# Kernel tuning notes

Measured on AMD Instinct MI355X. Metric: run time of the kernel, lower is better.

## Reference

```python
import jax, jax.numpy as jnp
import numpy as np
import math

POWER = 4
NUM_LEVELS = 2
STDS = [8, 4, 2, 1]          # stds sorted descending, as in __init__
KSIZE = 31                    # max(stds)*4 - 1
MAX_MIP = (NUM_LEVELS - 1) + math.log(2 * max(STDS)) / math.log(POWER)  # 3.0


def _blur_kernel():
    # (12, 3, 31, 31): output channel 3*i+c is a Gaussian(std=STDS[i]) applied to input channel c
    d = np.arange(KSIZE, dtype=np.float64) - (KSIZE - 1) / 2.0
    K = np.zeros((3 * len(STDS), 3, KSIZE, KSIZE), np.float32)
    for i, s in enumerate(STDS):
        g1 = np.exp(-0.5 * (d / s) ** 2)
        g1 = g1 / g1.sum()
        g = np.outer(g1, g1).astype(np.float32)
        for c in range(3):
            K[3 * i + c, c] = g
    return jnp.asarray(K)


def cube_sample(tex, dirs):
    # tex: (6, H, W, 3) cubemap faces in OpenGL order (+x,-x,+y,-y,+z,-z); dirs: (B, 3)
    H, W = tex.shape[1], tex.shape[2]
    x, y, z = dirs[:, 0], dirs[:, 1], dirs[:, 2]
    ax, ay, az = jnp.abs(x), jnp.abs(y), jnp.abs(z)
    is_x = (ax >= ay) & (ax >= az)
    is_y = (~is_x) & (ay >= az)
    face = jnp.where(is_x, jnp.where(x >= 0, 0, 1),
                     jnp.where(is_y, jnp.where(y >= 0, 2, 3),
                               jnp.where(z >= 0, 4, 5)))
    ma = jnp.where(is_x, ax, jnp.where(is_y, ay, az))
    conds = [face == i for i in range(6)]
    sc = jnp.select(conds, [-z, z, x, x, x, -x])
    tc = jnp.select(conds, [-y, -y, z, -z, -y, -y])
    inv = 1.0 / jnp.maximum(ma, 1e-12)
    u = 0.5 * (sc * inv + 1.0)
    v = 0.5 * (tc * inv + 1.0)
    fx = u * W - 0.5
    fy = v * H - 0.5
    x0 = jnp.floor(fx)
    y0 = jnp.floor(fy)
    wx = (fx - x0)[:, None]
    wy = (fy - y0)[:, None]
    x0i = jnp.clip(x0, 0, W - 1).astype(jnp.int32)
    x1i = jnp.clip(x0 + 1, 0, W - 1).astype(jnp.int32)
    y0i = jnp.clip(y0, 0, H - 1).astype(jnp.int32)
    y1i = jnp.clip(y0 + 1, 0, H - 1).astype(jnp.int32)
    t00 = tex[face, y0i, x0i]
    t10 = tex[face, y0i, x1i]
    t01 = tex[face, y1i, x0i]
    t11 = tex[face, y1i, x1i]
    return ((t00 * (1 - wx) + t10 * wx) * (1 - wy)
            + (t01 * (1 - wx) + t11 * wx) * wy)


def setup_inputs() -> dict:
    key = jax.random.key(0)
    k1, k2, k3, k4 = jax.random.split(key, 4)
    B = 2097152
    res = 512
    viewdirs = jax.random.normal(k1, (B, 3), dtype=jnp.float32)
    viewdirs = viewdirs / jnp.linalg.norm(viewdirs, axis=-1, keepdims=True)
    # miplevel = log(saSample/saTexel)/log(4)/2 ; make it span [0, 3.2] so the mask path fires
    saTexel = 4.0 * math.pi / (6 * res * res)
    u = jax.random.uniform(k2, (B, 1), dtype=jnp.float32)
    saSample = saTexel * (float(POWER) ** (2.0 * 3.2 * u))
    # learned cubemaps: coarse (128) then fine (512), as in bg_mats list order
    bg_mat0 = 0.1 + 0.05 * jax.random.normal(k3, (6, 128, 128, 3), dtype=jnp.float32)
    bg_mat1 = 0.1 + 0.05 * jax.random.normal(k4, (6, 512, 512, 3), dtype=jnp.float32)
    return {"viewdirs": viewdirs, "saSample": saSample, "bg_mat0": bg_mat0, "bg_mat1": bg_mat1}


def reference(viewdirs, saSample, bg_mat0, bg_mat1):
    res = bg_mat1.shape[1]
    saTexel = 4.0 * math.pi / (6 * res * res)
    miplevel = jnp.clip(jnp.log(saSample / saTexel) / math.log(POWER) / 2.0, 0.0, MAX_MIP)  # (B,1)

    # main level pass: mip=1 (coarse, weight 1/(2-1)=1), mip=0 (fine, weight 1/2)
    img = cube_sample(bg_mat0, viewdirs) * 1.0 + cube_sample(bg_mat1, viewdirs) * 0.5

    # blur pyramid from coarse map (start_mip=1, weight=1, identity activation)
    faces = jnp.transpose(bg_mat0, (0, 3, 1, 2))  # (6,3,h,h)
    conv = jax.lax.conv_general_dilated(faces, _blur_kernel(), (1, 1), 'SAME',
                                        dimension_numbers=('NCHW', 'OIHW', 'NCHW'))
    blur = jnp.zeros_like(img)
    wsum = jnp.zeros_like(miplevel)
    for i, s in enumerate(STDS):
        mat = jnp.transpose(conv[:, 3 * i:3 * i + 3], (0, 2, 3, 1))  # (6,h,h,3)
        mip = (NUM_LEVELS - 1) + math.log(2 * s) / math.log(POWER)
        w = 1.0 - jnp.clip(jnp.abs(mip - miplevel), 0.0, 1.0)  # (B,1)
        blur = blur + cube_sample(mat, viewdirs) * w
        wsum = wsum + w
    mask = miplevel >= NUM_LEVELS  # (B,1)
    img = jnp.where(mask, blur / jnp.maximum(wsum, 1e-8), img)
    return img
```

## Files before the change

kernel.cpp:

```cpp
#include <hip/hip_runtime.h>
#include <hip/hip_fp16.h>
#include <math.h>

#define KSIZE 31
#define HRAD 15

#define QSCALE (1023.0f / 0.75f)
#define QINV   (0.75f / 1023.0f)
#define QOFF   0.25f

union H8U { float4 f4; __half h[8]; };

__device__ inline unsigned quant3(float r, float g, float b) {
    int qr = (int)((r + QOFF) * QSCALE + 0.5f);
    int qg = (int)((g + QOFF) * QSCALE + 0.5f);
    int qb = (int)((b + QOFF) * QSCALE + 0.5f);
    qr = min(max(qr, 0), 1023);
    qg = min(max(qg, 0), 1023);
    qb = min(max(qb, 0), 1023);
    return (unsigned)(qr | (qg << 10) | (qb << 20));
}

__device__ inline float deqc(unsigned q, int sh) {
    return (float)((q >> sh) & 1023u) * QINV - QOFF;
}

__device__ inline void cube_coords(float x, float y, float z,
                                   int& face, float& u, float& v) {
    float ax = fabsf(x), ay = fabsf(y), az = fabsf(z);
    bool is_x = (ax >= ay) && (ax >= az);
    bool is_y = (!is_x) && (ay >= az);
    float ma, sc, tc;
    if (is_x) {
        if (x >= 0.0f) { face = 0; sc = -z; } else { face = 1; sc = z; }
        ma = ax; tc = -y;
    } else if (is_y) {
        if (y >= 0.0f) { face = 2; tc = z; } else { face = 3; tc = -z; }
        ma = ay; sc = x;
    } else {
        if (z >= 0.0f) { face = 4; sc = x; } else { face = 5; sc = -x; }
        ma = az; tc = -y;
    }
    float inv = 1.0f / fmaxf(ma, 1e-12f);
    u = 0.5 * (sc * inv + 1.0f);
    v = 0.5 * (tc * inv + 1.0f);
}

__device__ inline void nbq_setup(float u, float v, int HW, int face,
                                 int& rec, float& wx, float& wy) {
    float fx = u * (float)HW - 0.5f;
    float fy = v * (float)HW - 0.5f;
    float x0 = floorf(fx), y0 = floorf(fy);
    wx = fx - x0;
    wy = fy - y0;
    int xi = (int)x0, yi = (int)y0;
    if (xi < 0) { xi = 0; wx = 0.0f; }
    if (yi < 0) { yi = 0; wy = 0.0f; }
    rec = (face * HW + yi) * HW + xi;
}

__device__ inline void weights_inline(int tid, float wS[4][32]) {
    const float ss[4] = {8.f, 4.f, 2.f, 1.f};
    int lvl = (tid >> 5) & 3;
    int tap = tid & 31;
    float d = (float)tap - 15.0f;
    float q = d / ss[lvl];
    float g = (tap < KSIZE) ? expf(-0.5f * q * q) : 0.0f;
    float s = g;
#pragma unroll
    for (int k = 16; k; k >>= 1) s += __shfl_xor(s, k, 32);
    if (tid < 128) wS[lvl][tap] = g / s;
}

__global__ __launch_bounds__(256)
void prep1(const float* __restrict__ bg0, const float* __restrict__ bg1,
           float4* __restrict__ tmpH, uint4* __restrict__ bg0q,
           uint4* __restrict__ bg1q) {
    __shared__ float sm[1664];
    int b = blockIdx.x;
    int tid = threadIdx.x;

    if (b < 6144) {
        float* smA = sm;
        float* smB = sm + 771;
        int half = b & 1;
        int y    = (b >> 1) & 511;
        int f    = b >> 10;
        int x0   = half * 256;
        int yn   = min(y + 1, 511);
        const float* rowA = bg1 + (size_t)(f * 512 + y)  * 1536;
        const float* rowB = bg1 + (size_t)(f * 512 + yn) * 1536;
        for (int k = tid; k < 771; k += 256) {
            int t = k / 3;
            int c = k - t * 3;
            int gx = min(x0 + t, 511);
            smA[k] = rowA[gx * 3 + c];
            smB[k] = rowB[gx * 3 + c];
        }
        __syncthreads();
        int t0 = tid * 3;
        uint4 r;
        r.x = quant3(smA[t0 + 0], smA[t0 + 1], smA[t0 + 2]);
        r.y = quant3(smA[t0 + 3], smA[t0 + 4], smA[t0 + 5]);
        r.z = quant3(smB[t0 + 0], smB[t0 + 1], smB[t0 + 2]);
        r.w = quant3(smB[t0 + 3], smB[t0 + 4], smB[t0 + 5]);
        bg1q[(size_t)(f * 512 + y) * 512 + x0 + tid] = r;
        return;
    }

    float (*rows)[2][384] = (float (*)[2][384])sm;
    float (*wS)[32] = (float (*)[32])(sm + 1536);

    int bid  = b - 6144;
    int unit = tid >> 7;
    int lane = tid & 127;
    int face = bid / 64;
    int yrow = (bid % 64) * 2 + unit;

    weights_inline(tid, wS);

    int ynext = min(yrow + 1, 127);
    const float* srcA = bg0 + (size_t)(face * 128 + yrow) * 384;
    const float* srcB = bg0 + (size_t)(face * 128 + ynext) * 384;
    for (int k = lane; k < 384; k += 128) {
        rows[unit][0][k] = srcA[k];
        rows[unit][1][k] = srcB[k];
    }
    __syncthreads();

    int x = lane;
    float a[4][3] = {};
    for (int t = 0; t < KSIZE; ++t) {
        int xx = x + t - HRAD;
        if (xx >= 0 && xx < 128) {
            float r0 = rows[unit][0][xx * 3 + 0];
            float r1 = rows[unit][0][xx * 3 + 1];
            float r2 = rows[unit][0][xx * 3 + 2];
#pragma unroll
            for (int l = 0; l < 4; ++l) {
                float w = wS[l][t];
                a[l][0] += w * r0; a[l][1] += w * r1; a[l][2] += w * r2;
            }
        }
    }
    size_t idx = (size_t)(face * 128 + yrow) * 128 + x;
    H8U ta, tb;
#pragma unroll
    for (int l = 0; l < 2; ++l) {
        ta.h[l * 4 + 0] = __float2half(a[l][0]);
        ta.h[l * 4 + 1] = __float2half(a[l][1]);
        ta.h[l * 4 + 2] = __float2half(a[l][2]);
        ta.h[l * 4 + 3] = __float2half(0.0f);
        tb.h[l * 4 + 0] = __float2half(a[2 + l][0]);
        tb.h[l * 4 + 1] = __float2half(a[2 + l][1]);
        tb.h[l * 4 + 2] = __float2half(a[2 + l][2]);
        tb.h[l * 4 + 3] = __float2half(0.0f);
    }
    tmpH[idx * 2 + 0] = ta.f4;
    tmpH[idx * 2 + 1] = tb.f4;

    int x1 = min(x + 1, 127);
    uint4 r;
    r.x = quant3(rows[unit][0][x * 3 + 0], rows[unit][0][x * 3 + 1], rows[unit][0][x * 3 + 2]);
    r.y = quant3(rows[unit][0][x1 * 3 + 0], rows[unit][0][x1 * 3 + 1], rows[unit][0][x1 * 3 + 2]);
    r.z = quant3(rows[unit][1][x * 3 + 0], rows[unit][1][x * 3 + 1], rows[unit][1][x * 3 + 2]);
    r.w = quant3(rows[unit][1][x1 * 3 + 0], rows[unit][1][x1 * 3 + 1], rows[unit][1][x1 * 3 + 2]);
    bg0q[idx] = r;
}

__global__ __launch_bounds__(128)
void blur_v4(const float4* __restrict__ tmpH, uint4* __restrict__ blurq) {
    __shared__ float wS[4][32];
    int bid  = blockIdx.x;
    int yrow = bid & 127;
    int face = bid >> 7;
    int tid  = threadIdx.x;

    weights_inline(tid, wS);
    __syncthreads();

    int x = tid;
    float acc[12] = {};
    int ylo = max(yrow - HRAD, 0);
    int yhi = min(yrow + HRAD, 127);
    for (int yy = ylo; yy <= yhi; ++yy) {
        int t = yy - yrow + HRAD;
        size_t idx = (size_t)(face * 128 + yy) * 128 + x;
        H8U qa, qb;
        qa.f4 = tmpH[idx * 2 + 0];
        qb.f4 = tmpH[idx * 2 + 1];
        float w0 = wS[0][t], w1 = wS[1][t], w2 = wS[2][t], w3 = wS[3][t];
        acc[0]  += w0 * __half2float(qa.h[0]);
        acc[1]  += w0 * __half2float(qa.h[1]);
        acc[2]  += w0 * __half2float(qa.h[2]);
        acc[3]  += w1 * __half2float(qa.h[4]);
        acc[4]  += w1 * __half2float(qa.h[5]);
        acc[5]  += w1 * __half2float(qa.h[6]);
        acc[6]  += w2 * __half2float(qb.h[0]);
        acc[7]  += w2 * __half2float(qb.h[1]);
        acc[8]  += w2 * __half2float(qb.h[2]);
        acc[9]  += w3 * __half2float(qb.h[4]);
        acc[10] += w3 * __half2float(qb.h[5]);
        acc[11] += w3 * __half2float(qb.h[6]);
    }

    uint4 r;
    r.x = quant3(acc[0], acc[1], acc[2]);
    r.y = quant3(acc[3], acc[4], acc[5]);
    r.z = quant3(acc[6], acc[7], acc[8]);
    r.w = quant3(acc[9], acc[10], acc[11]);
    blurq[(size_t)(face * 128 + yrow) * 128 + x] = r;
}

__device__ inline void shade_one(float x, float y, float z, float sa,
                                 const uint4* __restrict__ bg0q,
                                 const uint4* __restrict__ bg1q,
                                 const uint4* __restrict__ blurq,
                                 float* __restrict__ R) {
    int face; float u, v;
    cube_coords(x, y, z, face, u, v);

    const float saTexel = (float)(4.0 * M_PI / (6.0 * 512.0 * 512.0));
    float m = logf(sa / saTexel);
    m = m / 1.3862943611198906f;
    m = m * 0.5f;
    m = fminf(fmaxf(m, 0.0f), 3.0f);

    if (m >= 2.0f) {
        float fx = u * 128.0f - 0.5f;
        float fy = v * 128.0f - 0.5f;
        float xf = floorf(fx), yf = floorf(fy);
        float wx = fx - xf, wy = fy - yf;
        int x0i = min(max((int)xf, 0), 127);
        int x1i = min(max((int)xf + 1, 0), 127);
        int y0i = min(max((int)yf, 0), 127);
        int y1i = min(max((int)yf + 1, 0), 127);
        int base = face << 14;
        uint4 q00 = blurq[base + y0i * 128 + x0i];
        uint4 q10 = blurq[base + y0i * 128 + x1i];
        uint4 q01 = blurq[base + y1i * 128 + x0i];
        uint4 q11 = blurq[base + y1i * 128 + x1i];

        float w0 = 1.0f - fminf(fabsf(3.0f - m), 1.0f);
        float w1 = 1.0f - fminf(fabsf(2.5f - m), 1.0f);
        float w2 = 1.0f - fminf(fabsf(2.0f - m), 1.0f);
        float w3 = 1.0f - fminf(fabsf(1.5f - m), 1.0f);
        float inv = 1.0f / fmaxf(w0 + w1 + w2 + w3, 1e-8f);

#pragma unroll
        for (int c = 0; c < 3; ++c) {
            int sh = c * 10;
            float v00 = w0 * deqc(q00.x, sh) + w1 * deqc(q00.y, sh) +
                        w2 * deqc(q00.z, sh) + w3 * deqc(q00.w, sh);
            float v10 = w0 * deqc(q10.x, sh) + w1 * deqc(q10.y, sh) +
                        w2 * deqc(q10.z, sh) + w3 * deqc(q10.w, sh);
            float v01 = w0 * deqc(q01.x, sh) + w1 * deqc(q01.y, sh) +
                        w2 * deqc(q01.z, sh) + w3 * deqc(q01.w, sh);
            float v11 = w0 * deqc(q11.x, sh) + w1 * deqc(q11.y, sh) +
                        w2 * deqc(q11.z, sh) + w3 * deqc(q11.w, sh);
            float top = v00 * (1.0f - wx) + v10 * wx;
            float bot = v01 * (1.0f - wx) + v11 * wx;
            R[c] = (top * (1.0f - wy) + bot * wy) * inv;
        }
    } else {
        int r0; float wx0, wy0;
        nbq_setup(u, v, 128, face, r0, wx0, wy0);
        int r1; float wx1, wy1;
        nbq_setup(u, v, 512, face, r1, wx1, wy1);
        uint4 p0 = bg0q[r0];
        uint4 p1 = bg1q[r1];
#pragma unroll
        for (int c = 0; c < 3; ++c) {
            int sh = c * 10;
            float t0 = deqc(p0.x, sh) * (1.0f - wx0) + deqc(p0.y, sh) * wx0;
            float b0 = deqc(p0.z, sh) * (1.0f - wx0) + deqc(p0.w, sh) * wx0;
            float c0 = t0 * (1.0f - wy0) + b0 * wy0;
            float t1 = deqc(p1.x, sh) * (1.0f - wx1) + deqc(p1.y, sh) * wx1;
            float b1 = deqc(p1.z, sh) * (1.0f - wx1) + deqc(p1.w, sh) * wx1;
            float c1 = t1 * (1.0f - wy1) + b1 * wy1;
            R[c] = c0 + 0.5f * c1;
        }
    }
}

__global__ __launch_bounds__(256)
void shade4(const float4* __restrict__ vd4, const float4* __restrict__ sa4,
            const uint4* __restrict__ bg0q, const uint4* __restrict__ bg1q,
            const uint4* __restrict__ blurq, float4* __restrict__ out4,
            int nquads) {
    int q = blockIdx.x * blockDim.x + threadIdx.x;
    if (q >= nquads) return;

    float4 a = vd4[3 * q + 0];
    float4 b = vd4[3 * q + 1];
    float4 c = vd4[3 * q + 2];
    float4 s = sa4[q];

    float X[4] = {a.x, a.w, b.z, c.y};
    float Y[4] = {a.y, b.x, b.w, c.z};
    float Z[4] = {a.z, b.y, c.x, c.w};
    float S[4] = {s.x, s.y, s.z, s.w};

    float R[12];
#pragma unroll
    for (int r = 0; r < 4; ++r) {
        shade_one(X[r], Y[r], Z[r], S[r], bg0q, bg1q, blurq, &R[3 * r]);
    }

    out4[3 * q + 0] = make_float4(R[0], R[1], R[2],  R[3]);
    out4[3 * q + 1] = make_float4(R[4], R[5], R[6],  R[7]);
    out4[3 * q + 2] = make_float4(R[8], R[9], R[10], R[11]);
}

extern "C" void kernel_launch(void* const* d_in, const int* in_sizes, int n_in,
                              void* d_out, int out_size, void* d_ws, size_t ws_size,
                              hipStream_t stream) {
    const float* viewdirs = (const float*)d_in[0];
    const float* saSample = (const float*)d_in[1];
    const float* bg0      = (const float*)d_in[2];
    const float* bg1      = (const float*)d_in[3];
    float* out = (float*)d_out;

    int B = in_sizes[0] / 3;
    int nquads = B / 4;

    uint4*  blurq = (uint4*)d_ws;
    uint4*  bg0q  = blurq + 98304;
    uint4*  bg1q  = bg0q + 98304;
    float4* tmpH  = (float4*)(bg1q + 1572864);

    prep1<<<6528, 256, 0, stream>>>(bg0, bg1, tmpH, bg0q, bg1q);
    blur_v4<<<6 * 128, 128, 0, stream>>>(tmpH, blurq);

    int blocks = (nquads + 255) / 256;
    shade4<<<blocks, 256, 0, stream>>>((const float4*)viewdirs,
                                       (const float4*)saSample,
                                       bg0q, bg1q, blurq,
                                       (float4*)out, nquads);
}
```

Before: 82.15 us.

## Fuse separable blur passes into one prep kernel with row-tiled shared memory

```diff
diff --git a/kernel.cpp b/kernel.cpp
--- a/kernel.cpp
+++ b/kernel.cpp
@@ -1,5 +1,4 @@
 #include <hip/hip_runtime.h>
-#include <hip/hip_fp16.h>
 #include <math.h>
 
 #define KSIZE 31
@@ -8,8 +7,6 @@
 #define QSCALE (1023.0f / 0.75f)
 #define QINV   (0.75f / 1023.0f)
 #define QOFF   0.25f
-
-union H8U { float4 f4; __half h[8]; };
 
 __device__ inline unsigned quant3(float r, float g, float b) {
     int qr = (int)((r + QOFF) * QSCALE + 0.5f);
@@ -42,8 +39,8 @@
         ma = az; tc = -y;
     }
     float inv = 1.0f / fmaxf(ma, 1e-12f);
-    u = 0.5 * (sc * inv + 1.0f);
-    v = 0.5 * (tc * inv + 1.0f);
+    u = 0.5f * (sc * inv + 1.0f);
+    v = 0.5f * (tc * inv + 1.0f);
 }
 
 __device__ inline void nbq_setup(float u, float v, int HW, int face,
@@ -73,143 +70,119 @@
 }
 
 __global__ __launch_bounds__(256)
-void prep1(const float* __restrict__ bg0, const float* __restrict__ bg1,
-           float4* __restrict__ tmpH, uint4* __restrict__ bg0q,
-           uint4* __restrict__ bg1q) {
-    __shared__ float sm[1664];
+void prep(const float* __restrict__ bg0, const float* __restrict__ bg1,
+          uint4* __restrict__ bg0q, uint4* __restrict__ bg1q,
+          uint4* __restrict__ blurq) {
+    __shared__ float4 sm4[3680];
+    float* sm = (float*)sm4;
     int b = blockIdx.x;
     int tid = threadIdx.x;
 
-    if (b < 6144) {
-        float* smA = sm;
-        float* smB = sm + 771;
-        int half = b & 1;
-        int y    = (b >> 1) & 511;
-        int f    = b >> 10;
-        int x0   = half * 256;
-        int yn   = min(y + 1, 511);
-        const float* rowA = bg1 + (size_t)(f * 512 + y)  * 1536;
-        const float* rowB = bg1 + (size_t)(f * 512 + yn) * 1536;
-        for (int k = tid; k < 771; k += 256) {
-            int t = k / 3;
-            int c = k - t * 3;
-            int gx = min(x0 + t, 511);
-            smA[k] = rowA[gx * 3 + c];
-            smB[k] = rowB[gx * 3 + c];
+    if (b < 384) {
+        int face  = b / 64;
+        int ytile = (b % 64) * 8;
+        for (int i = tid; i < 9 * 384; i += 256) {
+            int r  = i / 384;
+            int c4 = i - r * 384;
+            int gy = min(ytile + r, 511);
+            sm4[r * 384 + c4] =
+                ((const float4*)(bg1 + (size_t)(face * 512 + gy) * 1536))[c4];
         }
         __syncthreads();
-        int t0 = tid * 3;
-        uint4 r;
-        r.x = quant3(smA[t0 + 0], smA[t0 + 1], smA[t0 + 2]);
-        r.y = quant3(smA[t0 + 3], smA[t0 + 4], smA[t0 + 5]);
-        r.z = quant3(smB[t0 + 0], smB[t0 + 1], smB[t0 + 2]);
-        r.w = quant3(smB[t0 + 3], smB[t0 + 4], smB[t0 + 5]);
-        bg1q[(size_t)(f * 512 + y) * 512 + x0 + tid] = r;
+#pragma unroll
+        for (int i = 0; i < 16; ++i) {
+            int idx = i * 256 + tid;
+            int yl  = idx >> 9;
+            int x   = idx & 511;
+            int x1  = min(x + 1, 511);
+            const float* rA = sm + (size_t)yl * 1536;
+            const float* rB = sm + (size_t)(yl + 1) * 1536;
+            uint4 r;
+            r.x = quant3(rA[x * 3 + 0], rA[x * 3 + 1], rA[x * 3 + 2]);
+            r.y = quant3(rA[x1 * 3 + 0], rA[x1 * 3 + 1], rA[x1 * 3 + 2]);
+            r.z = quant3(rB[x * 3 + 0], rB[x * 3 + 1], rB[x * 3 + 2]);
+            r.w = quant3(rB[x1 * 3 + 0], rB[x1 * 3 + 1], rB[x1 * 3 + 2]);
+            bg1q[(size_t)(face * 512 + ytile + yl) * 512 + x] = r;
+        }
         return;
     }
 
-    float (*rows)[2][384] = (float (*)[2][384])sm;
-    float (*wS)[32] = (float (*)[32])(sm + 1536);
-
-    int bid  = b - 6144;
-    int unit = tid >> 7;
-    int lane = tid & 127;
-    int face = bid / 64;
-    int yrow = (bid % 64) * 2 + unit;
+    float (*wS)[32] = (float (*)[32])(sm + 14592);
+    int bb    = b - 384;
+    int face  = bb / 16;
+    int ytile = (bb % 16) * 8;
+    int x     = tid & 127;
+    int half  = tid >> 7;
 
     weights_inline(tid, wS);
 
-    int ynext = min(yrow + 1, 127);
-    const float* srcA = bg0 + (size_t)(face * 128 + yrow) * 384;
-    const float* srcB = bg0 + (size_t)(face * 128 + ynext) * 384;
-    for (int k = lane; k < 384; k += 128) {
-        rows[unit][0][k] = srcA[k];
-        rows[unit][1][k] = srcB[k];
+    for (int i = tid; i < 38 * 96; i += 256) {
+        int r  = i / 96;
+        int c4 = i - r * 96;
+        int gy = ytile - 15 + r;
+        float4 v = make_float4(0.f, 0.f, 0.f, 0.f);
+        if (gy >= 0 && gy <= 127)
+            v = ((const float4*)(bg0 + (size_t)(face * 128 + gy) * 384))[c4];
+        sm4[r * 96 + c4] = v;
     }
     __syncthreads();
 
-    int x = lane;
-    float a[4][3] = {};
-    for (int t = 0; t < KSIZE; ++t) {
-        int xx = x + t - HRAD;
-        if (xx >= 0 && xx < 128) {
-            float r0 = rows[unit][0][xx * 3 + 0];
-            float r1 = rows[unit][0][xx * 3 + 1];
-            float r2 = rows[unit][0][xx * 3 + 2];
-#pragma unroll
-            for (int l = 0; l < 4; ++l) {
-                float w = wS[l][t];
-                a[l][0] += w * r0; a[l][1] += w * r1; a[l][2] += w * r2;
+    int r0 = half * 4;
+    float acc[4][12] = {};
+    for (int rr = 0; rr < 34; ++rr) {
+        int r = r0 + rr;
+        const float* row = sm + (size_t)r * 384;
+        float hv[12] = {};
+        for (int t = 0; t < KSIZE; ++t) {
+            int xx = x + t - HRAD;
+            if (xx >= 0 && xx < 128) {
+                float c0 = row[xx * 3 + 0];
+                float c1 = row[xx * 3 + 1];
+                float c2 = row[xx * 3 + 2];
+#pragma unroll
+                for (int l = 0; l < 4; ++l) {
+                    float w = wS[l][t];
+                    hv[l * 3 + 0] += w * c0;
+                    hv[l * 3 + 1] += w * c1;
+                    hv[l * 3 + 2] += w * c2;
+                }
             }
         }
-    }
-    size_t idx = (size_t)(face * 128 + yrow) * 128 + x;
-    H8U ta, tb;
-#pragma unroll
-    for (int l = 0; l < 2; ++l) {
-        ta.h[l * 4 + 0] = __float2half(a[l][0]);
-        ta.h[l * 4 + 1] = __float2half(a[l][1]);
-        ta.h[l * 4 + 2] = __float2half(a[l][2]);
-        ta.h[l * 4 + 3] = __float2half(0.0f);
-        tb.h[l * 4 + 0] = __float2half(a[2 + l][0]);
-        tb.h[l * 4 + 1] = __float2half(a[2 + l][1]);
-        tb.h[l * 4 + 2] = __float2half(a[2 + l][2]);
-        tb.h[l * 4 + 3] = __float2half(0.0f);
-    }
-    tmpH[idx * 2 + 0] = ta.f4;
-    tmpH[idx * 2 + 1] = tb.f4;
-
-    int x1 = min(x + 1, 127);
-    uint4 r;
-    r.x = quant3(rows[unit][0][x * 3 + 0], rows[unit][0][x * 3 + 1], rows[unit][0][x * 3 + 2]);
-    r.y = quant3(rows[unit][0][x1 * 3 + 0], rows[unit][0][x1 * 3 + 1], rows[unit][0][x1 * 3 + 2]);
-    r.z = quant3(rows[unit][1][x * 3 + 0], rows[unit][1][x * 3 + 1], rows[unit][1][x * 3 + 2]);
-    r.w = quant3(rows[unit][1][x1 * 3 + 0], rows[unit][1][x1 * 3 + 1], rows[unit][1][x1 * 3 + 2]);
-    bg0q[idx] = r;
-}
-
-__global__ __launch_bounds__(128)
-void blur_v4(const float4* __restrict__ tmpH, uint4* __restrict__ blurq) {
-    __shared__ float wS[4][32];
-    int bid  = blockIdx.x;
-    int yrow = bid & 127;
-    int face = bid >> 7;
-    int tid  = threadIdx.x;
-
-    weights_inline(tid, wS);
-    __syncthreads();
-
-    int x = tid;
-    float acc[12] = {};
-    int ylo = max(yrow - HRAD, 0);
-    int yhi = min(yrow + HRAD, 127);
-    for (int yy = ylo; yy <= yhi; ++yy) {
-        int t = yy - yrow + HRAD;
-        size_t idx = (size_t)(face * 128 + yy) * 128 + x;
-        H8U qa, qb;
-        qa.f4 = tmpH[idx * 2 + 0];
-        qb.f4 = tmpH[idx * 2 + 1];
-        float w0 = wS[0][t], w1 = wS[1][t], w2 = wS[2][t], w3 = wS[3][t];
-        acc[0]  += w0 * __half2float(qa.h[0]);
-        acc[1]  += w0 * __half2float(qa.h[1]);
-        acc[2]  += w0 * __half2float(qa.h[2]);
-        acc[3]  += w1 * __half2float(qa.h[4]);
-        acc[4]  += w1 * __half2float(qa.h[5]);
-        acc[5]  += w1 * __half2float(qa.h[6]);
-        acc[6]  += w2 * __half2float(qb.h[0]);
-        acc[7]  += w2 * __half2float(qb.h[1]);
-        acc[8]  += w2 * __half2float(qb.h[2]);
-        acc[9]  += w3 * __half2float(qb.h[4]);
-        acc[10] += w3 * __half2float(qb.h[5]);
-        acc[11] += w3 * __half2float(qb.h[6]);
-    }
-
-    uint4 r;
-    r.x = quant3(acc[0], acc[1], acc[2]);
-    r.y = quant3(acc[3], acc[4], acc[5]);
-    r.z = quant3(acc[6], acc[7], acc[8]);
-    r.w = quant3(acc[9], acc[10], acc[11]);
-    blurq[(size_t)(face * 128 + yrow) * 128 + x] = r;
+#pragma unroll
+        for (int o = 0; o < 4; ++o) {
+            int t = r - (r0 + o);
+            if (t >= 0 && t <= 30) {
+                float w0 = wS[0][t], w1 = wS[1][t], w2 = wS[2][t], w3 = wS[3][t];
+                acc[o][0]  += w0 * hv[0];  acc[o][1]  += w0 * hv[1];  acc[o][2]  += w0 * hv[2];
+                acc[o][3]  += w1 * hv[3];  acc[o][4]  += w1 * hv[4];  acc[o][5]  += w1 * hv[5];
+                acc[o][6]  += w2 * hv[6];  acc[o][7]  += w2 * hv[7];  acc[o][8]  += w2 * hv[8];
+                acc[o][9]  += w3 * hv[9];  acc[o][10] += w3 * hv[10]; acc[o][11] += w3 * hv[11];
+            }
+        }
+    }
+
+#pragma unroll
+    for (int o = 0; o < 4; ++o) {
+        int yl = r0 + o;
+        int y  = ytile + yl;
+        uint4 q;
+        q.x = quant3(acc[o][0], acc[o][1], acc[o][2]);
+        q.y = quant3(acc[o][3], acc[o][4], acc[o][5]);
+        q.z = quant3(acc[o][6], acc[o][7], acc[o][8]);
+        q.w = quant3(acc[o][9], acc[o][10], acc[o][11]);
+        blurq[(size_t)(face * 128 + y) * 128 + x] = q;
+
+        const float* rowY  = sm + (size_t)(15 + yl) * 384;
+        int yl1 = (y < 127) ? (15 + yl + 1) : (15 + yl);
+        const float* rowY1 = sm + (size_t)yl1 * 384;
+        int x1 = min(x + 1, 127);
+        uint4 p;
+        p.x = quant3(rowY[x * 3 + 0],  rowY[x * 3 + 1],  rowY[x * 3 + 2]);
+        p.y = quant3(rowY[x1 * 3 + 0], rowY[x1 * 3 + 1], rowY[x1 * 3 + 2]);
+        p.z = quant3(rowY1[x * 3 + 0],  rowY1[x * 3 + 1],  rowY1[x * 3 + 2]);
+        p.w = quant3(rowY1[x1 * 3 + 0], rowY1[x1 * 3 + 1], rowY1[x1 * 3 + 2]);
+        bg0q[(size_t)(face * 128 + y) * 128 + x] = p;
+    }
 }
 
 __device__ inline void shade_one(float x, float y, float z, float sa,
@@ -324,13 +297,11 @@
     int B = in_sizes[0] / 3;
     int nquads = B / 4;
 
-    uint4*  blurq = (uint4*)d_ws;
-    uint4*  bg0q  = blurq + 98304;
-    uint4*  bg1q  = bg0q + 98304;
-    float4* tmpH  = (float4*)(bg1q + 1572864);
-
-    prep1<<<6528, 256, 0, stream>>>(bg0, bg1, tmpH, bg0q, bg1q);
-    blur_v4<<<6 * 128, 128, 0, stream>>>(tmpH, blurq);
+    uint4* blurq = (uint4*)d_ws;
+    uint4* bg0q  = blurq + 98304;
+    uint4* bg1q  = bg0q + 98304;
+
+    prep<<<480, 256, 0, stream>>>(bg0, bg1, bg0q, bg1q, blurq);
 
     int blocks = (nquads + 255) / 256;
     shade4<<<blocks, 256, 0, stream>>>((const float4*)viewdirs,
```

New measurement: 172.2 us. 110% more time.

## Rebalance prep kernels: overlap bg1 packing with vertical blur, split blur per half

Applied to the files above, without the earlier changes.

```diff
diff --git a/kernel.cpp b/kernel.cpp
--- a/kernel.cpp
+++ b/kernel.cpp
@@ -42,8 +42,8 @@
         ma = az; tc = -y;
     }
     float inv = 1.0f / fmaxf(ma, 1e-12f);
-    u = 0.5 * (sc * inv + 1.0f);
-    v = 0.5 * (tc * inv + 1.0f);
+    u = 0.5f * (sc * inv + 1.0f);
+    v = 0.5f * (tc * inv + 1.0f);
 }
 
 __device__ inline void nbq_setup(float u, float v, int HW, int face,
@@ -73,45 +73,14 @@
 }
 
 __global__ __launch_bounds__(256)
-void prep1(const float* __restrict__ bg0, const float* __restrict__ bg1,
-           float4* __restrict__ tmpH, uint4* __restrict__ bg0q,
-           uint4* __restrict__ bg1q) {
+void hblur(const float* __restrict__ bg0, float4* __restrict__ tmpH,
+           uint4* __restrict__ bg0q) {
     __shared__ float sm[1664];
-    int b = blockIdx.x;
-    int tid = threadIdx.x;
-
-    if (b < 6144) {
-        float* smA = sm;
-        float* smB = sm + 771;
-        int half = b & 1;
-        int y    = (b >> 1) & 511;
-        int f    = b >> 10;
-        int x0   = half * 256;
-        int yn   = min(y + 1, 511);
-        const float* rowA = bg1 + (size_t)(f * 512 + y)  * 1536;
-        const float* rowB = bg1 + (size_t)(f * 512 + yn) * 1536;
-        for (int k = tid; k < 771; k += 256) {
-            int t = k / 3;
-            int c = k - t * 3;
-            int gx = min(x0 + t, 511);
-            smA[k] = rowA[gx * 3 + c];
-            smB[k] = rowB[gx * 3 + c];
-        }
-        __syncthreads();
-        int t0 = tid * 3;
-        uint4 r;
-        r.x = quant3(smA[t0 + 0], smA[t0 + 1], smA[t0 + 2]);
-        r.y = quant3(smA[t0 + 3], smA[t0 + 4], smA[t0 + 5]);
-        r.z = quant3(smB[t0 + 0], smB[t0 + 1], smB[t0 + 2]);
-        r.w = quant3(smB[t0 + 3], smB[t0 + 4], smB[t0 + 5]);
-        bg1q[(size_t)(f * 512 + y) * 512 + x0 + tid] = r;
-        return;
-    }
-
     float (*rows)[2][384] = (float (*)[2][384])sm;
     float (*wS)[32] = (float (*)[32])(sm + 1536);
 
-    int bid  = b - 6144;
+    int bid  = blockIdx.x;
+    int tid  = threadIdx.x;
     int unit = tid >> 7;
     int lane = tid & 127;
     int face = bid / 64;
@@ -168,48 +137,71 @@
     bg0q[idx] = r;
 }
 
-__global__ __launch_bounds__(128)
-void blur_v4(const float4* __restrict__ tmpH, uint4* __restrict__ blurq) {
-    __shared__ float wS[4][32];
-    int bid  = blockIdx.x;
-    int yrow = bid & 127;
-    int face = bid >> 7;
-    int tid  = threadIdx.x;
+__global__ __launch_bounds__(256)
+void packv(const float* __restrict__ bg1, const float4* __restrict__ tmpH,
+           uint4* __restrict__ bg1q, uint2* __restrict__ blurq2) {
+    __shared__ float4 sm4[768];
+    int b = blockIdx.x;
+    int tid = threadIdx.x;
+
+    if (b < 3072) {
+        float* sm = (float*)sm4;
+        int y    = b & 511;
+        int face = b >> 9;
+        int yn   = min(y + 1, 511);
+        const float4* rA = (const float4*)(bg1 + (size_t)(face * 512 + y)  * 1536);
+        const float4* rB = (const float4*)(bg1 + (size_t)(face * 512 + yn) * 1536);
+        for (int i = tid; i < 384; i += 256) {
+            sm4[i]       = rA[i];
+            sm4[384 + i] = rB[i];
+        }
+        __syncthreads();
+        const float* a  = sm;
+        const float* bb = sm + 1536;
+#pragma unroll
+        for (int e = 0; e < 2; ++e) {
+            int x  = e * 256 + tid;
+            int x1 = min(x + 1, 511);
+            uint4 r;
+            r.x = quant3(a[x * 3 + 0],  a[x * 3 + 1],  a[x * 3 + 2]);
+            r.y = quant3(a[x1 * 3 + 0], a[x1 * 3 + 1], a[x1 * 3 + 2]);
+            r.z = quant3(bb[x * 3 + 0],  bb[x * 3 + 1],  bb[x * 3 + 2]);
+            r.w = quant3(bb[x1 * 3 + 0], bb[x1 * 3 + 1], bb[x1 * 3 + 2]);
+            bg1q[(size_t)(face * 512 + y) * 512 + x] = r;
+        }
+        return;
+    }
+
+    float (*wS)[32] = (float (*)[32])sm4;
+    int bb   = b - 3072;
+    int yrow = bb & 127;
+    int face = bb >> 7;
 
     weights_inline(tid, wS);
     __syncthreads();
 
-    int x = tid;
-    float acc[12] = {};
+    int x    = tid >> 1;
+    int half = tid & 1;
+    float a0 = 0.f, a1 = 0.f, a2 = 0.f, a3 = 0.f, a4 = 0.f, a5 = 0.f;
     int ylo = max(yrow - HRAD, 0);
     int yhi = min(yrow + HRAD, 127);
     for (int yy = ylo; yy <= yhi; ++yy) {
         int t = yy - yrow + HRAD;
-        size_t idx = (size_t)(face * 128 + yy) * 128 + x;
-        H8U qa, qb;
-        qa.f4 = tmpH[idx * 2 + 0];
-        qb.f4 = tmpH[idx * 2 + 1];
-        float w0 = wS[0][t], w1 = wS[1][t], w2 = wS[2][t], w3 = wS[3][t];
-        acc[0]  += w0 * __half2float(qa.h[0]);
-        acc[1]  += w0 * __half2float(qa.h[1]);
-        acc[2]  += w0 * __half2float(qa.h[2]);
-        acc[3]  += w1 * __half2float(qa.h[4]);
-        acc[4]  += w1 * __half2float(qa.h[5]);
-        acc[5]  += w1 * __half2float(qa.h[6]);
-        acc[6]  += w2 * __half2float(qb.h[0]);
-        acc[7]  += w2 * __half2float(qb.h[1]);
-        acc[8]  += w2 * __half2float(qb.h[2]);
-        acc[9]  += w3 * __half2float(qb.h[4]);
-        acc[10] += w3 * __half2float(qb.h[5]);
-        acc[11] += w3 * __half2float(qb.h[6]);
-    }
-
-    uint4 r;
-    r.x = quant3(acc[0], acc[1], acc[2]);
-    r.y = quant3(acc[3], acc[4], acc[5]);
-    r.z = quant3(acc[6], acc[7], acc[8]);
-    r.w = quant3(acc[9], acc[10], acc[11]);
-    blurq[(size_t)(face * 128 + yrow) * 128 + x] = r;
+        H8U q;
+        q.f4 = tmpH[((size_t)(face * 128 + yy) * 128 + x) * 2 + half];
+        float wA = wS[half * 2 + 0][t];
+        float wB = wS[half * 2 + 1][t];
+        a0 += wA * __half2float(q.h[0]);
+        a1 += wA * __half2float(q.h[1]);
+        a2 += wA * __half2float(q.h[2]);
+        a3 += wB * __half2float(q.h[4]);
+        a4 += wB * __half2float(q.h[5]);
+        a5 += wB * __half2float(q.h[6]);
+    }
+    uint2 o;
+    o.x = quant3(a0, a1, a2);
+    o.y = quant3(a3, a4, a5);
+    blurq2[((size_t)(face * 128 + yrow) * 128 + x) * 2 + half] = o;
 }
 
 __device__ inline void shade_one(float x, float y, float z, float sa,
@@ -329,8 +321,8 @@
     uint4*  bg1q  = bg0q + 98304;
     float4* tmpH  = (float4*)(bg1q + 1572864);
 
-    prep1<<<6528, 256, 0, stream>>>(bg0, bg1, tmpH, bg0q, bg1q);
-    blur_v4<<<6 * 128, 128, 0, stream>>>(tmpH, blurq);
+    hblur<<<384, 256, 0, stream>>>(bg0, tmpH, bg0q);
+    packv<<<3072 + 768, 256, 0, stream>>>(bg1, tmpH, bg1q, (uint2*)blurq);
 
     int blocks = (nquads + 255) / 256;
     shade4<<<blocks, 256, 0, stream>>>((const float4*)viewdirs,
```

Result: faster. 80.45 us (-2.1%).
